# Kernel tuning notes

Hardware: AMD Instinct MI355X
Metric: run time of the kernel (lower is better)

The kernel has to match this reference:

```python
import math
import jax, jax.numpy as jnp
import numpy as np

CANVAS_SHAPE = (256, 256)
NUM_SAMPLES = 32
MAX_LENGTH = 300.0
EPSILON = 1e-6


def _bezier_eval(cp, ts):
    # cp: [K, 2] control points, ts: [S] -> [S, 2] via Bernstein basis
    K = cp.shape[0]
    n = K - 1
    i = jnp.arange(K)
    binom = jnp.asarray([math.comb(n, k) for k in range(K)], dtype=cp.dtype)
    t = ts[:, None].astype(cp.dtype)  # [S, 1]
    basis = binom * (t ** i) * ((1.0 - t) ** (n - i))  # [S, K]
    return basis @ cp


def _decasteljau_left(cp, t):
    # Control points of the sub-curve on [0, t] (left de Casteljau subdivision).
    K = cp.shape[0]
    pts = cp
    left = [cp[0]]
    for _ in range(K - 1):
        pts = (1.0 - t) * pts[:-1] + t * pts[1:]
        left.append(pts[0])
    return jnp.stack(left)


def setup_inputs() -> dict:
    key = jax.random.key(0)
    k1, k2, k3 = jax.random.split(key, 3)
    B, K = 16, 4
    inputs = jax.random.uniform(k1, (B, K, 2), dtype=jnp.float32)  # normalized keypoints
    widths = jax.random.uniform(k2, (B,), dtype=jnp.float32) * 6.0 + 2.0  # stroke widths in px
    aa_factors = jax.random.uniform(k3, (B,), dtype=jnp.float32) * 2.0 + 1.0  # anti-alias exponents
    return {"inputs": inputs, "widths": widths, "aa_factors": aa_factors}


def reference(inputs, widths, aa_factors):
    H, W = CANVAS_SHAPE
    canvas_dims = jnp.asarray([H, W], dtype=inputs.dtype)
    key_points = inputs * canvas_dims[None, None, :]  # [B, K, 2]
    ts = jnp.linspace(0.0, 1.0, NUM_SAMPLES)

    def per_curve_samples(cp):
        # arc length approximated with NUM_SAMPLES piecewise-linear segments
        approx = _bezier_eval(cp, ts)  # [S, 2]
        seg = approx[1:] - approx[:-1]
        arc_len = jnp.sum(jnp.sqrt(jnp.sum(seg * seg, axis=-1)))
        # truncate curve to max_length if too long (no-op when arc_len <= MAX_LENGTH)
        t_trunc = jnp.minimum(1.0, MAX_LENGTH / (arc_len + EPSILON))
        cp_trunc = _decasteljau_left(cp, t_trunc)
        return _bezier_eval(cp_trunc, ts)  # [S, 2]

    sample_points = jax.vmap(per_curve_samples)(key_points)  # [B, S, 2]

    yy, xx = jnp.meshgrid(jnp.arange(H), jnp.arange(W), indexing="ij")
    positions = jnp.stack([yy, xx], axis=-1).reshape(-1, 2).astype(inputs.dtype)  # [HW, 2] as (y, x)

    # pairwise pixel-to-sample distances, min over samples (memory-bound reduction)
    diff = positions[None, None, :, :] - sample_points[:, :, None, :]  # [B, S, HW, 2]
    dists = jnp.sqrt(jnp.sum(diff * diff, axis=-1))  # [B, S, HW]
    min_d = jnp.min(dists, axis=1)  # [B, HW]

    canvas = 1.0 - (min_d / widths[:, None] + EPSILON) ** aa_factors[:, None]
    return jnp.clip(canvas, 0.0, 1.0).reshape(-1, H, W)
```

## Files before the change

### kernel.cpp

```cpp
#include <hip/hip_runtime.h>


constexpr int CH = 256, CW = 256;
constexpr int S = 32;
constexpr int NB = 16;
constexpr int BLK = 256;
constexpr int PPT = 4;
constexpr float MAXLEN = 300.0f;
constexpr float EPS = 1e-6f;

__device__ inline float2 bez4(const float2 cp[4], float t) {
    float u = 1.0f - t;
    float b0 = u * u * u;
    float b1 = 3.0f * u * u * t;
    float b2 = 3.0f * u * t * t;
    float b3 = t * t * t;
    float2 r;
    r.x = b0 * cp[0].x + b1 * cp[1].x + b2 * cp[2].x + b3 * cp[3].x;
    r.y = b0 * cp[0].y + b1 * cp[1].y + b2 * cp[2].y + b3 * cp[3].y;
    return r;
}

__device__ inline float shade(float m, float wd, float aa) {
    float md = sqrtf(m);
    float base = md / wd + EPS;
    float v = 1.0f - __expf(aa * __logf(base));
    return fminf(fmaxf(v, 0.0f), 1.0f);
}

__global__ __launch_bounds__(BLK) void curve_kernel(
    const float* __restrict__ inp,
    const float* __restrict__ widths,
    const float* __restrict__ aas,
    float* __restrict__ out)
{
    const int b = blockIdx.y;
    const int tid = threadIdx.x;

    __shared__ float2 s_samp[S];
    __shared__ float2 s_cp[4];

    float2 cp[4];
    if (tid < S) {
#pragma unroll
        for (int k = 0; k < 4; ++k) {
            cp[k].x = inp[(b * 4 + k) * 2 + 0] * 256.0f;
            cp[k].y = inp[(b * 4 + k) * 2 + 1] * 256.0f;
        }
        float t = (float)tid * (1.0f / 31.0f);
        s_samp[tid] = bez4(cp, t);
    }
    __syncthreads();

    if (tid == 0) {
        float arc = 0.0f;
        for (int j = 0; j < S - 1; ++j) {
            float dy = s_samp[j + 1].x - s_samp[j].x;
            float dx = s_samp[j + 1].y - s_samp[j].y;
            arc += sqrtf(dy * dy + dx * dx);
        }
        float tt = fminf(1.0f, MAXLEN / (arc + EPS));
        float u = 1.0f - tt;
        float2 a01, a12, a23, q0, q1, c0;
        a01.x = u * cp[0].x + tt * cp[1].x;  a01.y = u * cp[0].y + tt * cp[1].y;
        a12.x = u * cp[1].x + tt * cp[2].x;  a12.y = u * cp[1].y + tt * cp[2].y;
        a23.x = u * cp[2].x + tt * cp[3].x;  a23.y = u * cp[2].y + tt * cp[3].y;
        q0.x = u * a01.x + tt * a12.x;       q0.y = u * a01.y + tt * a12.y;
        q1.x = u * a12.x + tt * a23.x;       q1.y = u * a12.y + tt * a23.y;
        c0.x = u * q0.x + tt * q1.x;         c0.y = u * q0.y + tt * q1.y;
        s_cp[0] = cp[0]; s_cp[1] = a01; s_cp[2] = q0; s_cp[3] = c0;
    }
    __syncthreads();

    if (tid < S) {
        float2 cpl[4] = { s_cp[0], s_cp[1], s_cp[2], s_cp[3] };
        float t = (float)tid * (1.0f / 31.0f);
        s_samp[tid] = bez4(cpl, t);
    }
    __syncthreads();

    const float wd = widths[b];
    const float aa = aas[b];
    const int p0 = blockIdx.x * (BLK * PPT) + tid * PPT;
    const float fy = (float)(p0 >> 8);
    const float fx = (float)(p0 & 255);

    float m0 = 1e30f, m1 = 1e30f, m2 = 1e30f, m3 = 1e30f;
#pragma unroll
    for (int j = 0; j < S; ++j) {
        float2 sp = s_samp[j];
        float dy = fy - sp.x;
        float dy2 = dy * dy;
        float dx0 = fx - sp.y;
        float dx1 = fx + 1.0f - sp.y;
        float dx2 = fx + 2.0f - sp.y;
        float dx3 = fx + 3.0f - sp.y;
        m0 = fminf(m0, fmaf(dx0, dx0, dy2));
        m1 = fminf(m1, fmaf(dx1, dx1, dy2));
        m2 = fminf(m2, fmaf(dx2, dx2, dy2));
        m3 = fminf(m3, fmaf(dx3, dx3, dy2));
    }

    float4 o;
    o.x = shade(m0, wd, aa);
    o.y = shade(m1, wd, aa);
    o.z = shade(m2, wd, aa);
    o.w = shade(m3, wd, aa);
    *reinterpret_cast<float4*>(out + b * (CH * CW) + p0) = o;
}

extern "C" void kernel_launch(void* const* d_in, const int* in_sizes, int n_in,
                              void* d_out, int out_size, void* d_ws, size_t ws_size,
                              hipStream_t stream) {
    const float* inp = (const float*)d_in[0];
    const float* widths = (const float*)d_in[1];
    const float* aas = (const float*)d_in[2];
    float* out = (float*)d_out;

    dim3 grid((CH * CW) / (BLK * PPT), NB);
    curve_kernel<<<grid, BLK, 0, stream>>>(inp, widths, aas, out);
}
```

Before: 63.59 us.

## Tile canvas into 32x32 blocks and skip tiles far from the curve

Changes the grid from linear row strips to 2D 32x32 tiles per curve. Each block tests whether any sample point lies within stroke width of the tile's bounding box; if none do, the block writes zeros and returns without the distance loop. This relies on pixels farther than the width always clamping to zero, which holds since base>1 and aa>=1 gives a negative value. The per-block curve setup and extra ballot and sync are kept as overhead.

```diff
diff --git a/kernel.cpp b/kernel.cpp
--- a/kernel.cpp
+++ b/kernel.cpp
@@ -5,7 +5,7 @@
 constexpr int S = 32;
 constexpr int NB = 16;
 constexpr int BLK = 256;
-constexpr int PPT = 4;
+constexpr int TILE = 32;
 constexpr float MAXLEN = 300.0f;
 constexpr float EPS = 1e-6f;
 
@@ -34,11 +34,14 @@
     const float* __restrict__ aas,
     float* __restrict__ out)
 {
-    const int b = blockIdx.y;
+    const int b = blockIdx.z;
+    const int tx0 = blockIdx.x * TILE;
+    const int ty0 = blockIdx.y * TILE;
     const int tid = threadIdx.x;
 
     __shared__ float2 s_samp[S];
     __shared__ float2 s_cp[4];
+    __shared__ int s_active;
 
     float2 cp[4];
     if (tid < S) {
@@ -80,10 +83,30 @@
     __syncthreads();
 
     const float wd = widths[b];
+    bool pred = false;
+    if (tid < S) {
+        float2 sp = s_samp[tid];
+        float dyl = fmaxf(0.0f, fmaxf((float)ty0 - sp.x, sp.x - (float)(ty0 + TILE - 1)));
+        float dxl = fmaxf(0.0f, fmaxf((float)tx0 - sp.y, sp.y - (float)(tx0 + TILE - 1)));
+        pred = fmaf(dxl, dxl, dyl * dyl) < wd * wd;
+    }
+    unsigned long long mask = __ballot(pred);
+    if (tid == 0) s_active = (mask != 0ULL);
+    __syncthreads();
+
+    const int row = ty0 + (tid >> 3);
+    const int col = tx0 + (tid & 7) * 4;
+    float* dst = out + b * (CH * CW) + row * CW + col;
+
+    if (!s_active) {
+        float4 z = make_float4(0.0f, 0.0f, 0.0f, 0.0f);
+        *reinterpret_cast<float4*>(dst) = z;
+        return;
+    }
+
     const float aa = aas[b];
-    const int p0 = blockIdx.x * (BLK * PPT) + tid * PPT;
-    const float fy = (float)(p0 >> 8);
-    const float fx = (float)(p0 & 255);
+    const float fy = (float)row;
+    const float fx = (float)col;
 
     float m0 = 1e30f, m1 = 1e30f, m2 = 1e30f, m3 = 1e30f;
 #pragma unroll
@@ -106,7 +129,7 @@
     o.y = shade(m1, wd, aa);
     o.z = shade(m2, wd, aa);
     o.w = shade(m3, wd, aa);
-    *reinterpret_cast<float4*>(out + b * (CH * CW) + p0) = o;
+    *reinterpret_cast<float4*>(dst) = o;
 }
 
 extern "C" void kernel_launch(void* const* d_in, const int* in_sizes, int n_in,
@@ -117,6 +140,6 @@
     const float* aas = (const float*)d_in[2];
     float* out = (float*)d_out;
 
-    dim3 grid((CH * CW) / (BLK * PPT), NB);
+    dim3 grid(CW / TILE, CH / TILE, NB);
     curve_kernel<<<grid, BLK, 0, stream>>>(inp, widths, aas, out);
 }
```

Measured after the change: 63.19 us. About the same (-0.6%).
